# Performance work log

Hardware: AMD Instinct MI355X
Metric: run time of the kernel (lower is better)

Reference implementation:

```python
import jax, jax.numpy as jnp
import numpy as np

N_EMBD = 1024
N_HEAD = 16
HEAD_SIZE = N_EMBD // N_HEAD
B, T = 2, 2048
LN_EPS = 1e-5


def _layernorm(x, g, b):
    mu = jnp.mean(x, axis=-1, keepdims=True)
    var = jnp.var(x, axis=-1, keepdims=True)
    return (x - mu) * jax.lax.rsqrt(var + LN_EPS) * g + b


def setup_inputs() -> dict:
    key = jax.random.key(0)
    ks = jax.random.split(key, 12)
    s_in = 1.0 / np.sqrt(N_EMBD)
    s_ff = 1.0 / np.sqrt(4 * N_EMBD)
    return {
        "x": jax.random.normal(ks[0], (B, T, N_EMBD), jnp.float32),
        # per-head q/k/v linears stacked head-major: [n_embd, n_embd]
        "Wq": jax.random.uniform(ks[1], (N_EMBD, N_EMBD), jnp.float32, -s_in, s_in),
        "Wk": jax.random.uniform(ks[2], (N_EMBD, N_EMBD), jnp.float32, -s_in, s_in),
        "Wv": jax.random.uniform(ks[3], (N_EMBD, N_EMBD), jnp.float32, -s_in, s_in),
        "Wo": jax.random.uniform(ks[4], (N_EMBD, N_EMBD), jnp.float32, -s_in, s_in),
        "bo": jax.random.uniform(ks[5], (N_EMBD,), jnp.float32, -s_in, s_in),
        "W1": jax.random.uniform(ks[6], (N_EMBD, 4 * N_EMBD), jnp.float32, -s_in, s_in),
        "b1": jax.random.uniform(ks[7], (4 * N_EMBD,), jnp.float32, -s_in, s_in),
        "W2": jax.random.uniform(ks[8], (4 * N_EMBD, N_EMBD), jnp.float32, -s_ff, s_ff),
        "b2": jax.random.uniform(ks[9], (N_EMBD,), jnp.float32, -s_ff, s_ff),
        "g1": jnp.ones((N_EMBD,), jnp.float32),
        "be1": jnp.zeros((N_EMBD,), jnp.float32),
        "g2": jnp.ones((N_EMBD,), jnp.float32),
        "be2": jnp.zeros((N_EMBD,), jnp.float32),
    }


def reference(x, Wq, Wk, Wv, Wo, bo, W1, b1, W2, b2, g1, be1, g2, be2):
    Bx, Tx, C = x.shape
    # --- self-attention on ln1(x) ---
    h = _layernorm(x, g1, be1)
    q = (h @ Wq).reshape(Bx, Tx, N_HEAD, HEAD_SIZE)
    k = (h @ Wk).reshape(Bx, Tx, N_HEAD, HEAD_SIZE)
    v = (h @ Wv).reshape(Bx, Tx, N_HEAD, HEAD_SIZE)
    # NOTE: faithful to source -- scale uses full C (n_embd), not head_size
    scale = C ** (-0.5)
    wei = jnp.einsum("bqhd,bkhd->bhqk", q, k) * scale  # [B,H,T,T]
    causal = jnp.tril(jnp.ones((Tx, Tx), bool))
    wei = jnp.where(causal, wei, -jnp.inf)
    wei = jax.nn.softmax(wei, axis=-1)
    attn = jnp.einsum("bhqk,bkhd->bqhd", wei, v).reshape(Bx, Tx, C)
    x = x + (attn @ Wo + bo)
    # --- feed-forward on ln2(x) ---
    h2 = _layernorm(x, g2, be2)
    x = x + (jax.nn.relu(h2 @ W1 + b1) @ W2 + b2)
    return x
```

## Files before the change

kernel.cpp:

```cpp
#include <hip/hip_runtime.h>
#include <hip/hip_bf16.h>
#include <math.h>

#define BB 2
#define TT 2048
#define CC 1024
#define NH 16
#define HD 64
#define BT (BB*TT)
#define LN_EPS 1e-5f
#define ATT_SCALE 0.03125f

typedef __bf16 bf16x8 __attribute__((ext_vector_type(8)));
typedef __bf16 bf16x4 __attribute__((ext_vector_type(4)));
typedef short shortx4 __attribute__((ext_vector_type(4)));
typedef float floatx4 __attribute__((ext_vector_type(4)));

__device__ __forceinline__ void gl_lds16(const __bf16* g, __bf16* l) {
    __builtin_amdgcn_global_load_lds((const __attribute__((address_space(1))) void*)g,
                                     (__attribute__((address_space(3))) void*)l,
                                     16, 0, 0);
}

#define MFMA32(a, b, c) __builtin_amdgcn_mfma_f32_16x16x32_bf16(a, b, c, 0, 0, 0)

#if __has_builtin(__builtin_amdgcn_mfma_f32_16x16x16_bf16)
__device__ __forceinline__ floatx4 mfma16(bf16x4 a, bf16x4 b, floatx4 c) {
    return __builtin_amdgcn_mfma_f32_16x16x16_bf16(a, b, c, 0, 0, 0);
}
#else
__device__ __forceinline__ floatx4 mfma16(bf16x4 a, bf16x4 b, floatx4 c) {
    return __builtin_amdgcn_mfma_f32_16x16x16bf16_1k(
        __builtin_bit_cast(shortx4, a), __builtin_bit_cast(shortx4, b), c, 0, 0, 0);
}
#endif

#define BARRIER() __builtin_amdgcn_s_barrier()
#define MEMF()  asm volatile("" ::: "memory")
#define VM4()   asm volatile("s_waitcnt vmcnt(4)" ::: "memory")
#define VM0()   asm volatile("s_waitcnt vmcnt(0)" ::: "memory")

__device__ __forceinline__ void swizzle_xcd(int& xb, int& yb, int& zb) {
    int nx = gridDim.x, ny = gridDim.y;
    int total = nx * ny * (int)gridDim.z;
    int lin = blockIdx.x + nx * (blockIdx.y + ny * blockIdx.z);
    int c = lin & 7, s = lin >> 3;
    int idx = c * (total >> 3) + s;
    xb = idx % nx;
    yb = (idx / nx) % ny;
    zb = idx / (nx * ny);
}

__global__ __launch_bounds__(256) void transpose_ln(
        const float* __restrict__ Wq, const float* __restrict__ Wk,
        const float* __restrict__ Wv, const float* __restrict__ Wo,
        const float* __restrict__ W1, const float* __restrict__ W2,
        __bf16* __restrict__ WqkvT, __bf16* __restrict__ WoT,
        __bf16* __restrict__ W1T, __bf16* __restrict__ W2T,
        const float* __restrict__ x, const float* __restrict__ g1,
        const float* __restrict__ be1, __bf16* __restrict__ hb) {
    __shared__ float t[32][33];
    __shared__ float rs_[4], rss_[4];
    __shared__ float mu_s, inv_s;
    int idx = blockIdx.x;
    if (idx >= 12288) {
        int row = idx - 12288;
        const float4* xr = (const float4*)(x + (size_t)row * CC);
        float4 v = xr[threadIdx.x];
        float s  = v.x + v.y + v.z + v.w;
        float ss = v.x*v.x + v.y*v.y + v.z*v.z + v.w*v.w;
        #pragma unroll
        for (int off = 32; off; off >>= 1) {
            s  += __shfl_down(s, off);
            ss += __shfl_down(ss, off);
        }
        int lane = threadIdx.x & 63, wid = threadIdx.x >> 6;
        if (lane == 0) { rs_[wid] = s; rss_[wid] = ss; }
        __syncthreads();
        if (threadIdx.x == 0) {
            float S  = rs_[0] + rs_[1] + rs_[2] + rs_[3];
            float SS = rss_[0] + rss_[1] + rss_[2] + rss_[3];
            float mu  = S * (1.0f / CC);
            float var = SS * (1.0f / CC) - mu * mu;
            mu_s  = mu;
            inv_s = rsqrtf(var + LN_EPS);
        }
        __syncthreads();
        float mu = mu_s, inv = inv_s;
        float4 gv = ((const float4*)g1)[threadIdx.x];
        float4 bv = ((const float4*)be1)[threadIdx.x];
        bf16x4 o;
        o[0] = (__bf16)((v.x - mu) * inv * gv.x + bv.x);
        o[1] = (__bf16)((v.y - mu) * inv * gv.y + bv.y);
        o[2] = (__bf16)((v.z - mu) * inv * gv.z + bv.z);
        o[3] = (__bf16)((v.w - mu) * inv * gv.w + bv.w);
        *(bf16x4*)(hb + (size_t)row * CC + threadIdx.x * 4) = o;
        return;
    }
    const float* src; __bf16* dst; int K, N, tn, tk;
    if (idx < 3072) {
        int wsel = idx >> 10, local = idx & 1023;
        src = (wsel == 0) ? Wq : (wsel == 1 ? Wk : Wv);
        dst = WqkvT + (size_t)wsel * 1024 * 1024;
        K = 1024; N = 1024; tn = local & 31; tk = local >> 5;
    } else if (idx < 4096) {
        int local = idx - 3072;
        src = Wo; dst = WoT; K = 1024; N = 1024; tn = local & 31; tk = local >> 5;
    } else if (idx < 8192) {
        int local = idx - 4096;
        src = W1; dst = W1T; K = 1024; N = 4096; tn = local & 127; tk = local >> 7;
    } else {
        int local = idx - 8192;
        src = W2; dst = W2T; K = 4096; N = 1024; tn = local & 31; tk = local >> 5;
    }
    int n0 = tn * 32, k0 = tk * 32;
    int tx = threadIdx.x & 31, ty = threadIdx.x >> 5;
    #pragma unroll
    for (int r = ty; r < 32; r += 8)
        t[r][tx] = src[(size_t)(k0 + r) * N + n0 + tx];
    __syncthreads();
    #pragma unroll
    for (int r = ty; r < 32; r += 8)
        dst[(size_t)(n0 + r) * K + k0 + tx] = (__bf16)t[tx][r];
}

__global__ __launch_bounds__(256) void reduce_wo_ln(const __bf16* __restrict__ P,
                                                    const float* __restrict__ bo,
                                                    const float* __restrict__ x,
                                                    const float* __restrict__ g2,
                                                    const float* __restrict__ be2,
                                                    float* __restrict__ x2,
                                                    __bf16* __restrict__ hb) {
    int row = blockIdx.x;
    int c = threadIdx.x * 4;
    const size_t S = (size_t)BT * CC;
    float4 xb = *(const float4*)(x + (size_t)row * CC + c);
    float4 bb = *(const float4*)(bo + c);
    float4 v;
    v.x = xb.x + bb.x;
    v.y = xb.y + bb.y;
    v.z = xb.z + bb.z;
    v.w = xb.w + bb.w;
    #pragma unroll
    for (int z = 0; z < 4; ++z) {
        bf16x4 a = *(const bf16x4*)(P + z * S + (size_t)row * CC + c);
        v.x += (float)a[0]; v.y += (float)a[1]; v.z += (float)a[2]; v.w += (float)a[3];
    }
    *(float4*)(x2 + (size_t)row * CC + c) = v;

    float s  = v.x + v.y + v.z + v.w;
    float ss = v.x*v.x + v.y*v.y + v.z*v.z + v.w*v.w;
    #pragma unroll
    for (int off = 32; off; off >>= 1) {
        s  += __shfl_down(s, off);
        ss += __shfl_down(ss, off);
    }
    __shared__ float rs_[4], rss_[4];
    __shared__ float mu_s, inv_s;
    int lane = threadIdx.x & 63, wid = threadIdx.x >> 6;
    if (lane == 0) { rs_[wid] = s; rss_[wid] = ss; }
    __syncthreads();
    if (threadIdx.x == 0) {
        float S_  = rs_[0] + rs_[1] + rs_[2] + rs_[3];
        float SS = rss_[0] + rss_[1] + rss_[2] + rss_[3];
        float mu  = S_ * (1.0f / CC);
        float var = SS * (1.0f / CC) - mu * mu;
        mu_s  = mu;
        inv_s = rsqrtf(var + LN_EPS);
    }
    __syncthreads();
    float mu = mu_s, inv = inv_s;
    float4 gv = ((const float4*)g2)[threadIdx.x];
    float4 bv = ((const float4*)be2)[threadIdx.x];
    bf16x4 o;
    o[0] = (__bf16)((v.x - mu) * inv * gv.x + bv.x);
    o[1] = (__bf16)((v.y - mu) * inv * gv.y + bv.y);
    o[2] = (__bf16)((v.z - mu) * inv * gv.z + bv.z);
    o[3] = (__bf16)((v.w - mu) * inv * gv.w + bv.w);
    *(bf16x4*)(hb + (size_t)row * CC + c) = o;
}

__global__ __launch_bounds__(256) void reduce_ffn(const __bf16* __restrict__ P,
                                                  const float* __restrict__ b2,
                                                  const float* __restrict__ x2,
                                                  float* __restrict__ out) {
    int row = blockIdx.x;
    int c = threadIdx.x * 4;
    const size_t S = (size_t)BT * CC;
    float4 v = *(const float4*)(x2 + (size_t)row * CC + c);
    float4 bb = *(const float4*)(b2 + c);
    v.x += bb.x; v.y += bb.y; v.z += bb.z; v.w += bb.w;
    #pragma unroll
    for (int z = 0; z < 4; ++z) {
        bf16x4 a = *(const bf16x4*)(P + z * S + (size_t)row * CC + c);
        v.x += (float)a[0]; v.y += (float)a[1]; v.z += (float)a[2]; v.w += (float)a[3];
    }
    *(float4*)(out + (size_t)row * CC + c) = v;
}

__device__ __forceinline__ void stage_half(const __bf16* __restrict__ mat, int row0,
                                           int ldk, int k0, __bf16* lds, int tid) {
    int r = tid >> 3;
    int lch = (tid & 7) ^ (r & 7);
    const __bf16* gp = mat + (size_t)(row0 + r) * ldk + k0 + lch * 8;
    gl_lds16(gp, lds + tid * 8);
    gl_lds16(gp + (size_t)64 * ldk, lds + 4096 + tid * 8);
}

__device__ __forceinline__ void load_a(const __bf16* As_, int qr, int wr, int m, int g,
                                       bf16x8 (&fa)[4][2]) {
    #pragma unroll
    for (int i = 0; i < 4; ++i) {
        int ra = qr * 128 + wr * 64 + i * 16 + m;
        #pragma unroll
        for (int kk = 0; kk < 2; ++kk)
            fa[i][kk] = *(const bf16x8*)&As_[ra * 64 + (((kk * 4 + g) ^ (m & 7)) * 8)];
    }
}

__device__ __forceinline__ void load_b(const __bf16* Bs_, int qc, int wc, int m, int g,
                                       bf16x8 (&fb)[2][2]) {
    #pragma unroll
    for (int j = 0; j < 2; ++j) {
        int rb = qc * 128 + wc * 32 + j * 16 + m;
        #pragma unroll
        for (int kk = 0; kk < 2; ++kk)
            fb[j][kk] = *(const bf16x8*)&Bs_[rb * 64 + (((kk * 4 + g) ^ (m & 7)) * 8)];
    }
}

__device__ __forceinline__ void mfma_q(bf16x8 (&fa)[4][2], bf16x8 (&fb)[2][2],
                                       floatx4 (&a)[4][2]) {
    __builtin_amdgcn_s_setprio(1);
    #pragma unroll
    for (int i = 0; i < 4; ++i)
        #pragma unroll
        for (int j = 0; j < 2; ++j)
            #pragma unroll
            for (int kk = 0; kk < 2; ++kk)
                a[i][j] = MFMA32(fa[i][kk], fb[j][kk], a[i][j]);
    __builtin_amdgcn_s_setprio(0);
}

template<int SK, typename OT, bool BIAS, bool RELU, bool VSPLIT>
__global__ __launch_bounds__(512, 2) void gemm256(const __bf16* __restrict__ A,
                                                  const __bf16* __restrict__ Bt,
                                                  const float* __restrict__ bias,
                                                  OT* __restrict__ C,
                                                  __bf16* __restrict__ vt,
                                                  int M, int N, int K) {
    __shared__ __bf16 As[2][16384];
    __shared__ __bf16 Bs[2][16384];
    int bx, by, bz;
    swizzle_xcd(bx, by, bz);
    const int tid = threadIdx.x;
    const int l = tid & 63, w = tid >> 6;
    const int m = l & 15, g = l >> 4;
    const int wr = w >> 2, wc = w & 3;
    const int m0 = by * 256, n0 = bx * 256;
    const int Keff = K / SK;
    const int kb = (SK > 1) ? bz * Keff : 0;
    const int iters = Keff >> 7;

    floatx4 acc[2][2][4][2];
    #pragma unroll
    for (int a = 0; a < 2; ++a)
        #pragma unroll
        for (int b = 0; b < 2; ++b)
            #pragma unroll
            for (int i = 0; i < 4; ++i)
                #pragma unroll
                for (int j = 0; j < 2; ++j) {
                    floatx4 z = {0.f, 0.f, 0.f, 0.f};
                    acc[a][b][i][j] = z;
                }

    stage_half(A,  m0,       K, kb,      &As[0][0],    tid);
    stage_half(Bt, n0,       K, kb,      &Bs[0][0],    tid);
    stage_half(Bt, n0 + 128, K, kb,      &Bs[0][8192], tid);
    stage_half(A,  m0 + 128, K, kb,      &As[0][8192], tid);
    stage_half(A,  m0,       K, kb + 64, &As[1][0],    tid);
    stage_half(Bt, n0 + 128, K, kb + 64, &Bs[1][8192], tid);
    VM4(); BARRIER(); MEMF();

    bf16x8 fa[4][2], fbA[2][2], fbB[2][2];

    for (int it = 0; it < iters; ++it) {
        const bool lastI = (it == iters - 1);
        const int kB = kb + (2 * it + 1) * 64;
        const int kC = kB + 64;
        const int kD = kC + 64;

        load_a(&As[0][0], 0, wr, m, g, fa);
        load_b(&Bs[0][0], 0, wc, m, g, fbA);
        stage_half(Bt, n0, K, kB, &Bs[1][0], tid);
        MEMF(); BARRIER(); mfma_q(fa, fbA, acc[0][0]); BARRIER(); MEMF();
        load_b(&Bs[0][0], 1, wc, m, g, fbB);
        stage_half(A, m0 + 128, K, kB, &As[1][8192], tid);
        MEMF(); BARRIER(); mfma_q(fa, fbB, acc[0][1]); BARRIER(); MEMF();
        load_a(&As[0][0], 1, wr, m, g, fa);
        if (!lastI) stage_half(A, m0, K, kC, &As[0][0], tid);
        MEMF(); BARRIER(); mfma_q(fa, fbB, acc[1][1]); BARRIER(); MEMF();
        if (!lastI) { stage_half(Bt, n0 + 128, K, kC, &Bs[0][8192], tid);
                      VM4(); }
        else VM0();
        BARRIER(); mfma_q(fa, fbA, acc[1][0]); BARRIER(); MEMF();

        load_a(&As[1][0], 0, wr, m, g, fa);
        load_b(&Bs[1][0], 0, wc, m, g, fbA);
        if (!lastI) stage_half(Bt, n0, K, kC, &Bs[0][0], tid);
        MEMF(); BARRIER(); mfma_q(fa, fbA, acc[0][0]); BARRIER(); MEMF();
        load_b(&Bs[1][0], 1, wc, m, g, fbB);
        if (!lastI) stage_half(A, m0 + 128, K, kC, &As[0][8192], tid);
        MEMF(); BARRIER(); mfma_q(fa, fbB, acc[0][1]); BARRIER(); MEMF();
        load_a(&As[1][0], 1, wr, m, g, fa);
        if (!lastI) stage_half(A, m0, K, kD, &As[1][0], tid);
        MEMF(); BARRIER(); mfma_q(fa, fbB, acc[1][1]); BARRIER(); MEMF();
        if (!lastI) { stage_half(Bt, n0 + 128, K, kD, &Bs[1][8192], tid);
                      VM4(); }
        BARRIER(); mfma_q(fa, fbA, acc[1][0]); BARRIER(); MEMF();
    }

    if (SK > 1) {
        __bf16* P = (__bf16*)C + (size_t)bz * M * N;
        #pragma unroll
        for (int qr = 0; qr < 2; ++qr)
            #pragma unroll
            for (int i = 0; i < 4; ++i) {
                int row = m0 + qr * 128 + wr * 64 + i * 16 + g * 4;
                #pragma unroll
                for (int qc = 0; qc < 2; ++qc)
                    #pragma unroll
                    for (int j = 0; j < 2; ++j) {
                        int col = n0 + qc * 128 + wc * 32 + j * 16 + m;
                        #pragma unroll
                        for (int r = 0; r < 4; ++r)
                            P[(size_t)(row + r) * N + col] = (__bf16)acc[qr][qc][i][j][r];
                    }
            }
    } else if (VSPLIT && n0 >= 2048) {
        #pragma unroll
        for (int qr = 0; qr < 2; ++qr)
            #pragma unroll
            for (int i = 0; i < 4; ++i) {
                int row = m0 + qr * 128 + wr * 64 + i * 16 + g * 4;
                int bb = row >> 11, t0 = row & 2047;
                #pragma unroll
                for (int qc = 0; qc < 2; ++qc)
                    #pragma unroll
                    for (int j = 0; j < 2; ++j) {
                        int cv = n0 + qc * 128 + wc * 32 + j * 16 + m - 2048;
                        bf16x4 o;
                        #pragma unroll
                        for (int r = 0; r < 4; ++r) o[r] = (__bf16)acc[qr][qc][i][j][r];
                        *(bf16x4*)(vt + ((size_t)(bb * NH + (cv >> 6)) * HD + (cv & 63)) * 2048 + t0) = o;
                    }
            }
    } else {
        #pragma unroll
        for (int qr = 0; qr < 2; ++qr)
            #pragma unroll
            for (int i = 0; i < 4; ++i) {
                int row = m0 + qr * 128 + wr * 64 + i * 16 + g * 4;
                #pragma unroll
                for (int qc = 0; qc < 2; ++qc)
                    #pragma unroll
                    for (int j = 0; j < 2; ++j) {
                        int col = n0 + qc * 128 + wc * 32 + j * 16 + m;
                        float bv = BIAS ? bias[col] : 0.0f;
                        #pragma unroll
                        for (int r = 0; r < 4; ++r) {
                            float vo = acc[qr][qc][i][j][r] + bv;
                            if (RELU) vo = fmaxf(vo, 0.0f);
                            if (VSPLIT && col < 1024) vo *= ATT_SCALE;
                            C[(size_t)(row + r) * N + col] = (OT)vo;
                        }
                    }
            }
    }
}

__global__ __launch_bounds__(256, 4) void attn_mfma7(const __bf16* __restrict__ qkv,
                                                     const __bf16* __restrict__ vt,
                                                     __bf16* __restrict__ att) {
    const int p = blockIdx.x;
    const int h    = (p & 7) + 8 * ((p >> 7) & 1);
    const int q0   = (p >> 3) & 15;
    const int b    = (p >> 8) & 1;
    const int half = p >> 9;
    const int qs = half ? 31 - q0 : q0;

    const int tid = threadIdx.x;
    const int l = tid & 63, w = tid >> 6;
    const int m = l & 15, g = l >> 4;

    __shared__ __bf16 Ks[2][128][32];
    __shared__ __bf16 Vt3[8][64][16];

    const __bf16* qp = qkv + (size_t)b * TT * 3072 + h * HD;
    const __bf16* kp = qp + 1024;
    const __bf16* vh = vt + (size_t)(b * NH + h) * HD * 2048;

    bf16x8 qb0, qb1;
    {
        int qrow = qs * 64 + w * 16 + m;
        qb0 = *(const bf16x8*)(qp + (size_t)qrow * 3072 + g * 8);
        qb1 = *(const bf16x8*)(qp + (size_t)qrow * 3072 + 32 + g * 8);
    }

    floatx4 O[4];
    float l_s = 0.0f;
    #pragma unroll
    for (int jd = 0; jd < 4; ++jd) { floatx4 z = {0.f, 0.f, 0.f, 0.f}; O[jd] = z; }

    const int ktmax = qs >> 1;
    for (int kt = 0; kt <= ktmax; ++kt) {
        __syncthreads();
        #pragma unroll
        for (int c = 0; c < 4; ++c) {
            int idx = w * 4 + c;
            int dh = idx >> 3, k16 = idx & 7;
            gl_lds16(kp + (size_t)(kt * 128 + k16 * 16 + (l >> 2)) * 3072
                        + dh * 32 + (((l & 3) ^ ((l >> 3) & 3)) * 8),
                     (__bf16*)Ks + dh * 4096 + k16 * 512);
        }
        #pragma unroll
        for (int c = 0; c < 4; ++c) {
            int idx = w * 4 + c;
            int jt = idx >> 1, dhf = idx & 1;
            gl_lds16(vh + (size_t)(dhf * 32 + (l >> 1)) * 2048 + kt * 128
                        + jt * 16 + (((l & 1) ^ ((l >> 3) & 1)) * 8),
                     (__bf16*)Vt3 + jt * 1024 + dhf * 512);
        }
        __syncthreads();

        floatx4 S[8];
        #pragma unroll
        for (int jt = 0; jt < 8; ++jt) {
            int co = (g ^ ((m >> 1) & 3)) * 8;
            bf16x8 kf0 = *(const bf16x8*)&Ks[0][jt * 16 + m][co];
            bf16x8 kf1 = *(const bf16x8*)&Ks[1][jt * 16 + m][co];
            floatx4 z = {0.f, 0.f, 0.f, 0.f};
            z = MFMA32(kf0, qb0, z);
            S[jt] = MFMA32(kf1, qb1, z);
        }

        const bool last = (kt == ktmax);
        if (last) {
            int qr = (qs & 1) * 64 + w * 16 + m;
            #pragma unroll
            for (int jt = 0; jt < 8; ++jt)
                #pragma unroll
                for (int r = 0; r < 4; ++r)
                    if (jt * 16 + g * 4 + r > qr) S[jt][r] = -1e30f;
        }
        bf16x4 pv[8];
        #pragma unroll
        for (int jt = 0; jt < 8; ++jt) {
            bf16x4 t;
            #pragma unroll
            for (int r = 0; r < 4; ++r) {
                float p2 = __expf(S[jt][r]);
                l_s += p2;
                t[r] = (__bf16)p2;
            }
            pv[jt] = t;
        }

        #pragma unroll
        for (int jt = 0; jt < 8; ++jt)
            #pragma unroll
            for (int jd = 0; jd < 4; ++jd) {
                bf16x4 vf = *(const bf16x4*)&Vt3[jt][jd * 16 + m]
                                [((g >> 1) ^ ((m >> 2) & 1)) * 8 + (g & 1) * 4];
                O[jd] = mfma16(vf, pv[jt], O[jd]);
            }
    }

    float lsum = l_s;
    lsum += __shfl_xor(lsum, 16, 64);
    lsum += __shfl_xor(lsum, 32, 64);
    float inv = 1.0f / lsum;
    int qrow = qs * 64 + w * 16 + m;
    #pragma unroll
    for (int jd = 0; jd < 4; ++jd) {
        bf16x4 o;
        #pragma unroll
        for (int r = 0; r < 4; ++r) o[r] = (__bf16)(O[jd][r] * inv);
        *(bf16x4*)(att + ((size_t)b * TT + qrow) * CC + h * HD + jd * 16 + g * 4) = o;
    }
}

extern "C" void kernel_launch(void* const* d_in, const int* in_sizes, int n_in,
                              void* d_out, int out_size, void* d_ws, size_t ws_size,
                              hipStream_t stream) {
    const float* x   = (const float*)d_in[0];
    const float* Wq  = (const float*)d_in[1];
    const float* Wk  = (const float*)d_in[2];
    const float* Wv  = (const float*)d_in[3];
    const float* Wo  = (const float*)d_in[4];
    const float* bo  = (const float*)d_in[5];
    const float* W1  = (const float*)d_in[6];
    const float* b1  = (const float*)d_in[7];
    const float* W2  = (const float*)d_in[8];
    const float* b2  = (const float*)d_in[9];
    const float* g1  = (const float*)d_in[10];
    const float* be1 = (const float*)d_in[11];
    const float* g2  = (const float*)d_in[12];
    const float* be2 = (const float*)d_in[13];
    float* out = (float*)d_out;

    char* p = (char*)d_ws;
    char*   pool  = p;          p += (size_t)32 * 1024 * 1024;
    __bf16* qkvb  = (__bf16*)pool;
    __bf16* vtb   = (__bf16*)(pool + (size_t)BT * 3072 * 2);
    __bf16* wop   = (__bf16*)pool;
    __bf16* ffp   = (__bf16*)pool;
    __bf16* attb  = (__bf16*)p; p += (size_t)BT * CC * 2;
    __bf16* hb    = (__bf16*)p; p += (size_t)BT * CC * 2;
    float*  x2    = (float*)p;  p += (size_t)BT * CC * 4;
    __bf16* ffb   = (__bf16*)p; p += (size_t)BT * 4096 * 2;
    __bf16* WqkvT = (__bf16*)p; p += (size_t)3072 * 1024 * 2;
    __bf16* WoT   = (__bf16*)p; p += (size_t)1024 * 1024 * 2;
    __bf16* W1T   = (__bf16*)p; p += (size_t)4096 * 1024 * 2;
    __bf16* W2T   = (__bf16*)p; p += (size_t)1024 * 4096 * 2;

    transpose_ln<<<16384, 256, 0, stream>>>(Wq, Wk, Wv, Wo, W1, W2,
                                            WqkvT, WoT, W1T, W2T,
                                            x, g1, be1, hb);
    gemm256<1, __bf16, false, false, true><<<dim3(12, 16), 512, 0, stream>>>(
        hb, WqkvT, nullptr, qkvb, vtb, BT, 3072, 1024);
    attn_mfma7<<<1024, 256, 0, stream>>>(qkvb, vtb, attb);
    gemm256<4, __bf16, false, false, false><<<dim3(4, 16, 4), 512, 0, stream>>>(
        attb, WoT, nullptr, wop, nullptr, BT, 1024, 1024);
    reduce_wo_ln<<<BT, 256, 0, stream>>>(wop, bo, x, g2, be2, x2, hb);
    gemm256<1, __bf16, true, true, false><<<dim3(16, 16), 512, 0, stream>>>(
        hb, W1T, b1, ffb, nullptr, BT, 4096, 1024);
    gemm256<4, __bf16, false, false, false><<<dim3(4, 16, 4), 512, 0, stream>>>(
        ffb, W2T, nullptr, ffp, nullptr, BT, 1024, 4096);
    reduce_ffn<<<BT, 256, 0, stream>>>(ffp, b2, x2, out);
}
```

Measured before the change: 323.2 us.

## Replace split-K partial buffers with float atomic accumulation into residual outputs

The Wo and W2 split-K GEMMs now atomically add their fp32 partial tiles directly into the residual buffers (x2 seeded with x+bo, out seeded with x2+b2) instead of writing bf16 partials that a separate reduction kernel sums. The x+bo seed is folded into the first LN kernel, and the LN2 kernel becomes a seed kernel that also writes out. This removes the reduce_ffn kernel and the partial-buffer traffic. In exchange it adds atomic contention, makes the summation order nondeterministic, and relies on atomic throughput to global memory.

```diff
diff --git a/kernel.cpp b/kernel.cpp
--- a/kernel.cpp
+++ b/kernel.cpp
@@ -58,7 +58,8 @@
         __bf16* __restrict__ WqkvT, __bf16* __restrict__ WoT,
         __bf16* __restrict__ W1T, __bf16* __restrict__ W2T,
         const float* __restrict__ x, const float* __restrict__ g1,
-        const float* __restrict__ be1, __bf16* __restrict__ hb) {
+        const float* __restrict__ be1, __bf16* __restrict__ hb,
+        const float* __restrict__ bo, float* __restrict__ x2) {
     __shared__ float t[32][33];
     __shared__ float rs_[4], rss_[4];
     __shared__ float mu_s, inv_s;
@@ -67,6 +68,12 @@
         int row = idx - 12288;
         const float4* xr = (const float4*)(x + (size_t)row * CC);
         float4 v = xr[threadIdx.x];
+        float4 bov = ((const float4*)bo)[threadIdx.x];
+        float4 sx;
+        sx.x = v.x + bov.x; sx.y = v.y + bov.y;
+        sx.z = v.z + bov.z; sx.w = v.w + bov.w;
+        *(float4*)(x2 + (size_t)row * CC + threadIdx.x * 4) = sx;
+
         float s  = v.x + v.y + v.z + v.w;
         float ss = v.x*v.x + v.y*v.y + v.z*v.z + v.w*v.w;
         #pragma unroll
@@ -124,29 +131,20 @@
         dst[(size_t)(n0 + r) * K + k0 + tx] = (__bf16)t[tx][r];
 }
 
-__global__ __launch_bounds__(256) void reduce_wo_ln(const __bf16* __restrict__ P,
-                                                    const float* __restrict__ bo,
-                                                    const float* __restrict__ x,
-                                                    const float* __restrict__ g2,
-                                                    const float* __restrict__ be2,
-                                                    float* __restrict__ x2,
-                                                    __bf16* __restrict__ hb) {
+__global__ __launch_bounds__(256) void ln2_seed(const float* __restrict__ x2,
+                                                const float* __restrict__ b2,
+                                                const float* __restrict__ g2,
+                                                const float* __restrict__ be2,
+                                                float* __restrict__ outs,
+                                                __bf16* __restrict__ hb) {
     int row = blockIdx.x;
     int c = threadIdx.x * 4;
-    const size_t S = (size_t)BT * CC;
-    float4 xb = *(const float4*)(x + (size_t)row * CC + c);
-    float4 bb = *(const float4*)(bo + c);
-    float4 v;
-    v.x = xb.x + bb.x;
-    v.y = xb.y + bb.y;
-    v.z = xb.z + bb.z;
-    v.w = xb.w + bb.w;
-    #pragma unroll
-    for (int z = 0; z < 4; ++z) {
-        bf16x4 a = *(const bf16x4*)(P + z * S + (size_t)row * CC + c);
-        v.x += (float)a[0]; v.y += (float)a[1]; v.z += (float)a[2]; v.w += (float)a[3];
-    }
-    *(float4*)(x2 + (size_t)row * CC + c) = v;
+    float4 v = *(const float4*)(x2 + (size_t)row * CC + c);
+    float4 bb = *(const float4*)(b2 + c);
+    float4 o2;
+    o2.x = v.x + bb.x; o2.y = v.y + bb.y;
+    o2.z = v.z + bb.z; o2.w = v.w + bb.w;
+    *(float4*)(outs + (size_t)row * CC + c) = o2;
 
     float s  = v.x + v.y + v.z + v.w;
     float ss = v.x*v.x + v.y*v.y + v.z*v.z + v.w*v.w;
@@ -180,24 +178,6 @@
     *(bf16x4*)(hb + (size_t)row * CC + c) = o;
 }
 
-__global__ __launch_bounds__(256) void reduce_ffn(const __bf16* __restrict__ P,
-                                                  const float* __restrict__ b2,
-                                                  const float* __restrict__ x2,
-                                                  float* __restrict__ out) {
-    int row = blockIdx.x;
-    int c = threadIdx.x * 4;
-    const size_t S = (size_t)BT * CC;
-    float4 v = *(const float4*)(x2 + (size_t)row * CC + c);
-    float4 bb = *(const float4*)(b2 + c);
-    v.x += bb.x; v.y += bb.y; v.z += bb.z; v.w += bb.w;
-    #pragma unroll
-    for (int z = 0; z < 4; ++z) {
-        bf16x4 a = *(const bf16x4*)(P + z * S + (size_t)row * CC + c);
-        v.x += (float)a[0]; v.y += (float)a[1]; v.z += (float)a[2]; v.w += (float)a[3];
-    }
-    *(float4*)(out + (size_t)row * CC + c) = v;
-}
-
 __device__ __forceinline__ void stage_half(const __bf16* __restrict__ mat, int row0,
                                            int ldk, int k0, __bf16* lds, int tid) {
     int r = tid >> 3;
@@ -242,7 +222,7 @@
     __builtin_amdgcn_s_setprio(0);
 }
 
-template<int SK, typename OT, bool BIAS, bool RELU, bool VSPLIT>
+template<int SK, typename OT, bool BIAS, bool RELU, bool VSPLIT, bool ATOM>
 __global__ __launch_bounds__(512, 2) void gemm256(const __bf16* __restrict__ A,
                                                   const __bf16* __restrict__ Bt,
                                                   const float* __restrict__ bias,
@@ -321,7 +301,25 @@
         BARRIER(); mfma_q(fa, fbA, acc[1][0]); BARRIER(); MEMF();
     }
 
-    if (SK > 1) {
+    if (SK > 1 && ATOM) {
+        float* P = (float*)C;
+        #pragma unroll
+        for (int qr = 0; qr < 2; ++qr)
+            #pragma unroll
+            for (int i = 0; i < 4; ++i) {
+                int row = m0 + qr * 128 + wr * 64 + i * 16 + g * 4;
+                #pragma unroll
+                for (int qc = 0; qc < 2; ++qc)
+                    #pragma unroll
+                    for (int j = 0; j < 2; ++j) {
+                        int col = n0 + qc * 128 + wc * 32 + j * 16 + m;
+                        #pragma unroll
+                        for (int r = 0; r < 4; ++r)
+                            unsafeAtomicAdd(&P[(size_t)(row + r) * N + col],
+                                            acc[qr][qc][i][j][r]);
+                    }
+            }
+    } else if (SK > 1) {
         __bf16* P = (__bf16*)C + (size_t)bz * M * N;
         #pragma unroll
         for (int qr = 0; qr < 2; ++qr)
@@ -514,8 +512,6 @@
     char*   pool  = p;          p += (size_t)32 * 1024 * 1024;
     __bf16* qkvb  = (__bf16*)pool;
     __bf16* vtb   = (__bf16*)(pool + (size_t)BT * 3072 * 2);
-    __bf16* wop   = (__bf16*)pool;
-    __bf16* ffp   = (__bf16*)pool;
     __bf16* attb  = (__bf16*)p; p += (size_t)BT * CC * 2;
     __bf16* hb    = (__bf16*)p; p += (size_t)BT * CC * 2;
     float*  x2    = (float*)p;  p += (size_t)BT * CC * 4;
@@ -527,16 +523,15 @@
 
     transpose_ln<<<16384, 256, 0, stream>>>(Wq, Wk, Wv, Wo, W1, W2,
                                             WqkvT, WoT, W1T, W2T,
-                                            x, g1, be1, hb);
-    gemm256<1, __bf16, false, false, true><<<dim3(12, 16), 512, 0, stream>>>(
+                                            x, g1, be1, hb, bo, x2);
+    gemm256<1, __bf16, false, false, true, false><<<dim3(12, 16), 512, 0, stream>>>(
         hb, WqkvT, nullptr, qkvb, vtb, BT, 3072, 1024);
     attn_mfma7<<<1024, 256, 0, stream>>>(qkvb, vtb, attb);
-    gemm256<4, __bf16, false, false, false><<<dim3(4, 16, 4), 512, 0, stream>>>(
-        attb, WoT, nullptr, wop, nullptr, BT, 1024, 1024);
-    reduce_wo_ln<<<BT, 256, 0, stream>>>(wop, bo, x, g2, be2, x2, hb);
-    gemm256<1, __bf16, true, true, false><<<dim3(16, 16), 512, 0, stream>>>(
+    gemm256<4, float, false, false, false, true><<<dim3(4, 16, 4), 512, 0, stream>>>(
+        attb, WoT, nullptr, x2, nullptr, BT, 1024, 1024);
+    ln2_seed<<<BT, 256, 0, stream>>>(x2, b2, g2, be2, out, hb);
+    gemm256<1, __bf16, true, true, false, false><<<dim3(16, 16), 512, 0, stream>>>(
         hb, W1T, b1, ffb, nullptr, BT, 4096, 1024);
-    gemm256<4, __bf16, false, false, false><<<dim3(4, 16, 4), 512, 0, stream>>>(
-        ffb, W2T, nullptr, ffp, nullptr, BT, 1024, 4096);
-    reduce_ffn<<<BT, 256, 0, stream>>>(ffp, b2, x2, out);
-}
+    gemm256<4, float, false, false, false, true><<<dim3(4, 16, 4), 512, 0, stream>>>(
+        ffb, W2T, nullptr, out, nullptr, BT, 1024, 4096);
+}
```

Result: slower. 387.0 us (+19.7%).
